# Kernel tuning notes

Measured on AMD Instinct MI355X. Metric: run time of the kernel, lower is better.

The kernel has to match this reference:

```python
import jax, jax.numpy as jnp
import numpy as np
from jax import lax
from jax.scipy.special import logsumexp

GW_WEIGHT = 20.0
GAMMA_P = 0.01
IN_ITER = 5
OUT_ITER = 10
LAMBDA_STEP = 0.01
N1, N2, D = 2048, 2048, 128
EMB_SCALE = 0.05  # keeps exp(-x@x.T) numerically sane, mimics trained embeddings
ADJ_DENSITY = 0.005


def setup_inputs() -> dict:
    key = jax.random.key(0)
    k1, k2, k3, k4 = jax.random.split(key, 4)
    out1 = jax.random.normal(k1, (N1, D), jnp.float32) * EMB_SCALE
    out2 = jax.random.normal(k2, (N2, D), jnp.float32) * EMB_SCALE

    def make_adj(k, n):
        m = (jax.random.uniform(k, (n, n)) < ADJ_DENSITY).astype(jnp.float32)
        m = jnp.maximum(m, m.T)                      # symmetric, like to_dense_adj of undirected graph
        return m * (1.0 - jnp.eye(n, dtype=jnp.float32))

    adj1 = make_adj(k3, N1)
    adj2 = make_adj(k4, N2)
    threshold_lambda = jnp.float32(1.0 / (N1 * N2))  # init_lambda / (n1*n2)
    return {"out1": out1, "out2": out2, "adj1": adj1, "adj2": adj2,
            "threshold_lambda": threshold_lambda}


def sinkhorn_stable(inter_c, intra_c1, intra_c2, gw_weight, gamma_p, lam,
                    in_iter, out_iter):
    """Log-domain (stabilized) entropic GW Sinkhorn.
    Outer loop: linearize the GW cost around current plan s (shifted by lam);
    inner loop: stabilized Sinkhorn with uniform marginals."""
    n1, n2 = inter_c.shape
    dt = inter_c.dtype
    log_mu = jnp.full((n1,), -np.log(n1), dt)
    log_nu = jnp.full((n2,), -np.log(n2), dt)
    c1sq = intra_c1 ** 2
    c2sq = intra_c2 ** 2
    s0 = jnp.full((n1, n2), 1.0 / (n1 * n2), dt)

    def outer_body(_, s):
        s_hat = s - lam
        a = jnp.sum(s_hat, axis=1)                    # [n1]
        b = jnp.sum(s_hat, axis=0)                    # [n2]
        # GW cost linearization: c1^2 a 1^T + 1 b^T c2^2 - 2 c1 s c2^T
        gw_cost = ((c1sq @ a)[:, None] + (b @ c2sq)[None, :]
                   - 2.0 * (intra_c1 @ s_hat @ intra_c2.T))
        cost = inter_c + gw_weight * gw_cost
        K = -cost / gamma_p                           # log kernel

        def inner_body(_, uv):
            u, v = uv
            u = log_mu - logsumexp(K + v[None, :], axis=1)
            v = log_nu - logsumexp(K + u[:, None], axis=0)
            return (u, v)

        u, v = lax.fori_loop(0, in_iter, inner_body,
                             (jnp.zeros((n1,), dt), jnp.zeros((n2,), dt)))
        return jnp.exp(K + u[:, None] + v[None, :])

    return lax.fori_loop(0, out_iter, outer_body, s0)


def _update_lambda(inter_c, intra_c1, intra_c2, s, gw_weight):
    # mid = c1^2 @ 1 * n2 + 1 @ c2^2 * n1 - 2 c1 @ 1 @ c2^T is rank-structured;
    # compute sum(mid*s) and sum(mid) without materializing mid.
    n1, n2 = inter_c.shape
    c1sq = intra_c1 ** 2
    c2sq = intra_c2 ** 2
    r1sq = jnp.sum(c1sq, axis=1)      # rowsum of c1^2  [n1]
    c2s = jnp.sum(c2sq, axis=0)       # colsum of c2^2  [n2]
    rs1 = jnp.sum(intra_c1, axis=1)   # [n1]
    rs2 = jnp.sum(intra_c2, axis=1)   # [n2]
    a_s = jnp.sum(s, axis=1)
    b_s = jnp.sum(s, axis=0)
    k1 = jnp.sum(inter_c)
    k2 = n2 * (r1sq @ a_s) + n1 * (c2s @ b_s) - 2.0 * (rs1 @ (s @ rs2))
    k3 = (n2 * n2) * jnp.sum(r1sq) + (n1 * n1) * jnp.sum(c2s) \
         - 2.0 * jnp.sum(rs1) * jnp.sum(rs2)
    return (k1 + 2.0 * gw_weight * k2) / (2.0 * gw_weight * k3)


def reference(out1, out2, adj1, adj2, threshold_lambda):
    n1, n2 = out1.shape[0], out2.shape[0]
    inter_c = jnp.exp(-(out1 @ out2.T))
    intra_c1 = jnp.exp(-(out1 @ out1.T)) * adj1
    intra_c2 = jnp.exp(-(out2 @ out2.T)) * adj2

    # torch.no_grad() block
    s = sinkhorn_stable(inter_c, intra_c1, intra_c2, GW_WEIGHT, GAMMA_P,
                        threshold_lambda, IN_ITER, OUT_ITER)
    lam = (LAMBDA_STEP * _update_lambda(inter_c, intra_c1, intra_c2, s, GW_WEIGHT)
           + (1.0 - LAMBDA_STEP) * threshold_lambda)

    s_hat = s - lam
    w_loss = jnp.sum(inter_c * s_hat)
    a = jnp.sum(s_hat, axis=1)
    b = jnp.sum(s_hat, axis=0)
    c1sq = intra_c1 ** 2
    c2sq = intra_c2 ** 2
    gw_loss = jnp.sum(((c1sq @ a)[:, None] + (b @ c2sq)[None, :]
                       - 2.0 * (intra_c1 @ s_hat @ intra_c2.T)) * s_hat)
    loss = w_loss + GW_WEIGHT * gw_loss + 20.0
    return (loss, s, lam)
```

## Files before the change

kernel.cpp:

```cpp
#include <hip/hip_runtime.h>
#include <math.h>

#define N 2048
#define DIM 128
#define CAP (N*64)
#define LOGN 7.6246189861593985f

typedef unsigned long long u64;
typedef unsigned int u32;
typedef unsigned short u16;

__device__ __forceinline__ u32 bf16bits(float f) {
  u32 x = __float_as_uint(f);
  return (x + 0x7fffu + ((x >> 16) & 1u)) >> 16;
}
__device__ __forceinline__ u32 pack_bf16x2(float lo, float hi) {
  return bf16bits(lo) | (bf16bits(hi) << 16);
}
__device__ __forceinline__ float bflo(u32 u) { return __uint_as_float(u << 16); }
__device__ __forceinline__ float bfhi(u32 u) { return __uint_as_float(u & 0xffff0000u); }


__global__ __launch_bounds__(256) void k_gemm_inter(
    const float* __restrict__ A, const float* __restrict__ B,
    float* __restrict__ O, double* __restrict__ k1p) {
  __shared__ __align__(16) float As[64][65];
  __shared__ __align__(16) float Bs[64][65];
  __shared__ float red[256];
  const int t = threadIdx.x;
  const int i0 = blockIdx.y * 64, j0 = blockIdx.x * 64;
  const int tx = t & 15, ty = t >> 4;
  float acc[4][4] = {};
  for (int kk = 0; kk < DIM; kk += 64) {
    if (kk) __syncthreads();
    for (int q = t; q < 64 * 16; q += 256) {
      int row = q >> 4, k4 = (q & 15) << 2;
      float4 av = *(const float4*)&A[(size_t)(i0 + row) * DIM + kk + k4];
      As[k4 + 0][row] = av.x; As[k4 + 1][row] = av.y;
      As[k4 + 2][row] = av.z; As[k4 + 3][row] = av.w;
      float4 bv = *(const float4*)&B[(size_t)(j0 + row) * DIM + kk + k4];
      Bs[k4 + 0][row] = bv.x; Bs[k4 + 1][row] = bv.y;
      Bs[k4 + 2][row] = bv.z; Bs[k4 + 3][row] = bv.w;
    }
    __syncthreads();
    #pragma unroll 4
    for (int k = 0; k < 64; ++k) {
      float av[4], bv[4];
      #pragma unroll
      for (int d = 0; d < 4; ++d) { av[d] = As[k][ty * 4 + d]; bv[d] = Bs[k][tx * 4 + d]; }
      #pragma unroll
      for (int di = 0; di < 4; ++di)
        #pragma unroll
        for (int dj = 0; dj < 4; ++dj)
          acc[di][dj] = fmaf(av[di], bv[dj], acc[di][dj]);
    }
  }
  float psum = 0.f;
  #pragma unroll
  for (int di = 0; di < 4; ++di)
    #pragma unroll
    for (int dj = 0; dj < 4; ++dj) {
      float vv = __expf(-acc[di][dj]);
      O[(size_t)(i0 + ty * 4 + di) * N + (j0 + tx * 4 + dj)] = vv;
      psum += vv;
    }
  red[t] = psum; __syncthreads();
  for (int off = 128; off; off >>= 1) { if (t < off) red[t] += red[t + off]; __syncthreads(); }
  if (t == 0) k1p[blockIdx.y * 32 + blockIdx.x] = (double)red[0];
}

__global__ __launch_bounds__(256) void k_count(const float* __restrict__ adj, int* __restrict__ cnt) {
  int i = blockIdx.x * 4 + (threadIdx.x >> 6);
  int lane = threadIdx.x & 63;
  const float* row = adj + (size_t)i * N;
  int c = 0;
  for (int j = lane; j < N; j += 64) c += (row[j] != 0.f) ? 1 : 0;
  for (int off = 32; off; off >>= 1) c += __shfl_down(c, off);
  if (lane == 0) cnt[i] = c;
}

__global__ __launch_bounds__(256) void k_scan(const int* __restrict__ cnt, int* __restrict__ rp) {
  __shared__ int sums[256];
  int t = threadIdx.x;
  int local[8]; int run = 0;
  int base = t * 8;
  #pragma unroll
  for (int k = 0; k < 8; ++k) { local[k] = run; run += cnt[base + k]; }
  sums[t] = run; __syncthreads();
  for (int off = 1; off < 256; off <<= 1) {
    int val = (t >= off) ? sums[t - off] : 0;
    __syncthreads();
    sums[t] += val;
    __syncthreads();
  }
  int pre = (t == 0) ? 0 : sums[t - 1];
  #pragma unroll
  for (int k = 0; k < 8; ++k) rp[base + k] = pre + local[k];
  if (t == 255) rp[N] = sums[255];
}

__global__ __launch_bounds__(256) void k_fill(const float* __restrict__ adj, const int* __restrict__ rp,
                                              int* __restrict__ cols, int* __restrict__ rows) {
  int i = blockIdx.x * 4 + (threadIdx.x >> 6);
  int lane = threadIdx.x & 63;
  const float* row = adj + (size_t)i * N;
  int pos = rp[i];
  for (int j0 = 0; j0 < N; j0 += 64) {
    bool p = row[j0 + lane] != 0.f;
    u64 mask = __ballot(p);
    if (p) {
      int off = __popcll(mask & ((1ull << lane) - 1ull));
      cols[pos + off] = j0 + lane;
      rows[pos + off] = i;
    }
    pos += __popcll(mask);
  }
}

__global__ __launch_bounds__(256) void k_vals(const int* __restrict__ rp, const int* __restrict__ rows,
                                              const int* __restrict__ cols, float* __restrict__ vals,
                                              const float* __restrict__ emb) {
  int lane = threadIdx.x & 63;
  int total = rp[N];
  for (int p = blockIdx.x * 4 + (threadIdx.x >> 6); p < total; p += 8192) {
    int i = rows[p], k = cols[p];
    const float* ei = emb + (size_t)i * DIM;
    const float* ek = emb + (size_t)k * DIM;
    float s = ei[lane] * ek[lane] + ei[lane + 64] * ek[lane + 64];
    for (int off = 32; off; off >>= 1) s += __shfl_down(s, off);
    if (lane == 0) vals[p] = __expf(-s);
  }
}

__global__ __launch_bounds__(256) void k_rowstats(const int* __restrict__ rp, const float* __restrict__ vals,
                                                  float* __restrict__ rs, float* __restrict__ rsq) {
  int i = blockIdx.x * 4 + (threadIdx.x >> 6);
  int lane = threadIdx.x & 63;
  int p0 = rp[i], p1 = rp[i + 1];
  float s1 = 0.f, s2 = 0.f;
  for (int p = p0 + lane; p < p1; p += 64) { float w = vals[p]; s1 += w; s2 += w * w; }
  for (int off = 32; off; off >>= 1) { s1 += __shfl_down(s1, off); s2 += __shfl_down(s2, off); }
  if (lane == 0) { rs[i] = s1; rsq[i] = s2; }
}

template<int V>
__global__ __launch_bounds__(256) void k_spmmt(const int* __restrict__ rp, const int* __restrict__ cols,
                                               const float* __restrict__ vals, const u32* __restrict__ S,
                                               const float* __restrict__ af, const float* __restrict__ bf,
                                               u16* __restrict__ Out) {
  __shared__ int winc[512];
  __shared__ float winv[512];
  __shared__ int rb[5];
  const int t = threadIdx.x;
  const int tile = blockIdx.x & 3;
  const int cu = tile * 256 + t;
  const int i0 = (blockIdx.x >> 2) * 4;
  const int p0 = rp[i0];
  if (t < 5) rb[t] = rp[i0 + t] - p0;
  __syncthreads();
  const int nn = rb[4];
  for (int k = t; k < nn; k += 256) {
    int col = cols[p0 + k];
    winc[k] = col << 10;
    winv[k] = (V == 0) ? vals[p0 + k] * af[col] : vals[p0 + k];
  }
  __syncthreads();
  float alo[4], ahi[4];
  #pragma unroll
  for (int r = 0; r < 4; ++r) {
    int pe = rb[r + 1], p = rb[r];
    float l0 = 0.f, l1 = 0.f, h0 = 0.f, h1 = 0.f;
    for (; p + 1 < pe; p += 2) {
      u32 u0 = S[winc[p] + cu], u1 = S[winc[p + 1] + cu];
      l0 = fmaf(winv[p],     bflo(u0), l0);  h0 = fmaf(winv[p],     bfhi(u0), h0);
      l1 = fmaf(winv[p + 1], bflo(u1), l1);  h1 = fmaf(winv[p + 1], bfhi(u1), h1);
    }
    if (p < pe) {
      u32 u = S[winc[p] + cu];
      l0 = fmaf(winv[p], bflo(u), l0);  h0 = fmaf(winv[p], bfhi(u), h0);
    }
    alo[r] = l0 + l1; ahi[r] = h0 + h1;
  }
  const int c0 = cu * 2;
  if (V == 0) {
    float2 bv = *(const float2*)&bf[c0];
    #pragma unroll
    for (int r = 0; r < 4; ++r) { alo[r] *= bv.x; ahi[r] *= bv.y; }
  }
  u32* O32 = (u32*)Out;
  *(uint2*)&O32[(size_t)c0 * 1024 + (i0 >> 1)] =
      make_uint2(pack_bf16x2(alo[0], alo[1]), pack_bf16x2(alo[2], alo[3]));
  *(uint2*)&O32[(size_t)(c0 + 1) * 1024 + (i0 >> 1)] =
      make_uint2(pack_bf16x2(ahi[0], ahi[1]), pack_bf16x2(ahi[2], ahi[3]));
}

template<int MODE>
__global__ __launch_bounds__(256) void k_iter(
    u32* __restrict__ P,
    const float* __restrict__ inter, const u32* __restrict__ M32,
    const int* __restrict__ rp1, const int* __restrict__ cols1, const float* __restrict__ vals1,
    const float* __restrict__ r1sq, const float* __restrict__ rs1,
    const float* __restrict__ r2sq, const float* __restrict__ rs2,
    const float* __restrict__ lamp, const float* __restrict__ asv_in,
    const float* __restrict__ bvec, float* __restrict__ avec,
    float* __restrict__ part) {
  __shared__ u32 Pl[4 * 1024];
  __shared__ float bl[N];
  __shared__ float a4[4];
  const int t = threadIdx.x;
  const int r0 = blockIdx.x * 4;
  const int w = t >> 6, lane = t & 63;
  const int row = r0 + w;

  if (MODE == 0) {
    #pragma unroll
    for (int q = 0; q < 2; ++q) {
      int j = (q * 256 + t) * 4;
      *(float4*)&bl[j] = *(const float4*)&bvec[j];
    }
    #pragma unroll
    for (int q = 0; q < 4; ++q) {
      int g = (q * 256 + t) * 4;
      *(uint4*)&Pl[g] = *(const uint4*)&P[(size_t)r0 * 1024 + g];
    }
    __syncthreads();
    float y = 0.f;
    const u32* Pr = Pl + w * 1024;
    #pragma unroll
    for (int k = 0; k < 16; ++k) {
      int g = lane + k * 64;
      u32 u = Pr[g];
      y = fmaf(bflo(u), bl[2 * g], y);
      y = fmaf(bfhi(u), bl[2 * g + 1], y);
    }
    for (int off = 32; off; off >>= 1) y += __shfl_xor(y, off);
    if (lane == 0) { float aw = 1.f / (2048.f * y); a4[w] = aw; avec[row] = aw; }
  } else {
    const float lam = *lamp;
    const float f = 0.00048828125f - lam * 2048.f;
    float ai_, rli;
    if (MODE == 2) {
      ai_ = -2000.f * r1sq[row] * f;
      rli = 4000.f * rs1[row] * (2.384185791015625e-07f - lam);
    } else {
      int q0 = rp1[row], q1 = rp1[row + 1];
      float acc = 0.f;
      for (int p = q0 + lane; p < q1; p += 64) {
        float wv = vals1[p];
        acc = fmaf(wv * wv, asv_in[cols1[p]], acc);
      }
      for (int off = 32; off; off >>= 1) acc += __shfl_xor(acc, off);
      ai_ = -2000.f * (acc - lam * 2048.f * r1sq[row]);
      rli = -4000.f * lam * rs1[row];
    }
    const float bjf = -2000.f * f;
    float kv[32];
    float m = -INFINITY;
    const float* ir = inter + (size_t)row * N;
    const u32* mr = M32 + (size_t)row * 1024;
    #pragma unroll
    for (int q = 0; q < 8; ++q) {
      int j = lane * 4 + q * 256;
      float4 iv = *(const float4*)&ir[j];
      float4 rq = *(const float4*)&r2sq[j];
      float4 r2 = *(const float4*)&rs2[j];
      float k0 = fmaf(-100.f, iv.x, fmaf(bjf, rq.x, ai_ + rli * r2.x));
      float k1 = fmaf(-100.f, iv.y, fmaf(bjf, rq.y, ai_ + rli * r2.y));
      float k2 = fmaf(-100.f, iv.z, fmaf(bjf, rq.z, ai_ + rli * r2.z));
      float k3 = fmaf(-100.f, iv.w, fmaf(bjf, rq.w, ai_ + rli * r2.w));
      if (MODE == 1) {
        uint2 mu = *(const uint2*)&mr[j >> 1];
        k0 = fmaf(4000.f, bflo(mu.x), k0);
        k1 = fmaf(4000.f, bfhi(mu.x), k1);
        k2 = fmaf(4000.f, bflo(mu.y), k2);
        k3 = fmaf(4000.f, bfhi(mu.y), k3);
      }
      kv[q * 4 + 0] = k0; kv[q * 4 + 1] = k1; kv[q * 4 + 2] = k2; kv[q * 4 + 3] = k3;
      m = fmaxf(m, fmaxf(fmaxf(k0, k1), fmaxf(k2, k3)));
    }
    for (int off = 32; off; off >>= 1) m = fmaxf(m, __shfl_xor(m, off));
    float ss = 0.f;
    #pragma unroll
    for (int q = 0; q < 8; ++q) {
      float p0 = __expf(kv[q * 4 + 0] - m);
      float p1 = __expf(kv[q * 4 + 1] - m);
      float p2 = __expf(kv[q * 4 + 2] - m);
      float p3 = __expf(kv[q * 4 + 3] - m);
      ss += (p0 + p1) + (p2 + p3);
      u32 lo = pack_bf16x2(p0, p1), hi = pack_bf16x2(p2, p3);
      int g = lane * 2 + q * 128;
      Pl[w * 1024 + g] = lo; Pl[w * 1024 + g + 1] = hi;
      *(uint2*)&P[(size_t)row * 1024 + g] = make_uint2(lo, hi);
    }
    for (int off = 32; off; off >>= 1) ss += __shfl_xor(ss, off);
    if (lane == 0) { float aw = 1.f / (2048.f * ss); a4[w] = aw; avec[row] = aw; }
  }
  __syncthreads();
  const float a0 = a4[0], a1 = a4[1], a2 = a4[2], a3 = a4[3];
  #pragma unroll
  for (int k = 0; k < 4; ++k) {
    int g = k * 256 + t;
    u32 u0 = Pl[g], u1 = Pl[1024 + g], u2 = Pl[2048 + g], u3 = Pl[3072 + g];
    float zlo = bflo(u0) * a0 + bflo(u1) * a1 + bflo(u2) * a2 + bflo(u3) * a3;
    float zhi = bfhi(u0) * a0 + bfhi(u1) * a1 + bfhi(u2) * a2 + bfhi(u3) * a3;
    *(float2*)&part[(size_t)blockIdx.x * N + 2 * g] = make_float2(zlo, zhi);
  }
}

__global__ __launch_bounds__(256) void k_comb(const float* __restrict__ part, float* __restrict__ bvec) {
  __shared__ float pp[16][17];
  const int t = threadIdx.x;
  const int cl = t & 15, kg = t >> 4;
  const int c = blockIdx.x * 16 + cl;
  float z = 0.f;
  for (int k = kg * 32; k < kg * 32 + 32; ++k) z += part[(size_t)k * N + c];
  pp[kg][cl] = z;
  __syncthreads();
  if (t < 16) {
    float zz = 0.f;
    #pragma unroll
    for (int g = 0; g < 16; ++g) zz += pp[g][t];
    bvec[blockIdx.x * 16 + t] = 1.f / (2048.f * zz);
  }
}

__global__ __launch_bounds__(256) void k_rowfin(const u32* __restrict__ P, const float* __restrict__ bvec,
                                                const float* __restrict__ avec, float* __restrict__ as_) {
  __shared__ float bl[N];
  const int t = threadIdx.x;
  #pragma unroll
  for (int q = 0; q < 2; ++q) {
    int j = (q * 256 + t) * 4;
    *(float4*)&bl[j] = *(const float4*)&bvec[j];
  }
  __syncthreads();
  const int w = t >> 6, lane = t & 63;
  const int row = blockIdx.x * 4 + w;
  const u32* Pr = P + (size_t)row * 1024;
  float y = 0.f;
  #pragma unroll
  for (int k = 0; k < 16; ++k) {
    int g = lane + k * 64;
    u32 u = Pr[g];
    y = fmaf(bflo(u), bl[2 * g], y);
    y = fmaf(bfhi(u), bl[2 * g + 1], y);
  }
  for (int off = 32; off; off >>= 1) y += __shfl_xor(y, off);
  if (lane == 0) as_[row] = avec[row] * y;
}


__global__ __launch_bounds__(256) void k_prep2(
    const int* __restrict__ rp1, const int* __restrict__ cols1, const float* __restrict__ vals1,
    const float* __restrict__ r2sq, const float* __restrict__ as_,
    float* __restrict__ paf, float* __restrict__ pbf) {
  int g = blockIdx.x * 256 + threadIdx.x;
  if (g < N) {
    int p0 = rp1[g], p1 = rp1[g + 1];
    float acc = 0.f;
    for (int p = p0; p < p1; ++p) { float w = vals1[p]; acc = fmaf(w * w, as_[cols1[p]], acc); }
    paf[g] = acc;
  } else {
    int j = g - N;
    pbf[j] = r2sq[j] * 0.00048828125f;
  }
}

__global__ __launch_bounds__(256) void k_fstats(
    const float* __restrict__ inter, const u32* __restrict__ P, const u32* __restrict__ M32,
    const float* __restrict__ rs2, const float* __restrict__ avec, const float* __restrict__ bvec,
    float* __restrict__ sOut, float* __restrict__ sisr, float* __restrict__ yv,
    double* __restrict__ dotp) {
  __shared__ __align__(16) float r2[N];
  __shared__ __align__(16) float bl[N];
  __shared__ double redm[4];
  const int t = threadIdx.x;
  #pragma unroll
  for (int q = 0; q < 2; ++q) {
    int j = (q * 256 + t) * 4;
    *(float4*)&r2[j] = *(const float4*)&rs2[j];
    *(float4*)&bl[j] = *(const float4*)&bvec[j];
  }
  __syncthreads();
  const int w = t >> 6, lane = t & 63;
  const int row = blockIdx.x * 4 + w;
  const float av = avec[row];
  const float* ir = inter + (size_t)row * N;
  const u32* mr = M32 + (size_t)row * 1024;
  const u32* Pr = P + (size_t)row * 1024;
  float* sr = sOut + (size_t)row * N;
  float d1 = 0.f, d2 = 0.f;
  double dm = 0.0;
  #pragma unroll 4
  for (int k = 0; k < 16; ++k) {
    int g = lane + k * 64;
    int j = 2 * g;
    u32 u = Pr[g];
    u32 mu = mr[g];
    float s0 = bflo(u) * av * bl[j];
    float s1 = bfhi(u) * av * bl[j + 1];
    float2 iv = *(const float2*)&ir[j];
    sr[j] = s0; sr[j + 1] = s1;
    d1 += iv.x * s0 + iv.y * s1;
    d2 += s0 * r2[j] + s1 * r2[j + 1];
    dm += (double)(bflo(mu) * s0) + (double)(bfhi(mu) * s1);
  }
  for (int off = 32; off; off >>= 1) {
    d1 += __shfl_down(d1, off);
    d2 += __shfl_down(d2, off);
    dm += __shfl_down(dm, off);
  }
  if (lane == 0) { sisr[row] = d1; yv[row] = d2; redm[w] = dm; }
  __syncthreads();
  if (t == 0) dotp[blockIdx.x] = redm[0] + redm[1] + redm[2] + redm[3];
}

__global__ __launch_bounds__(256) void k_final(
    const float* __restrict__ paf, const float* __restrict__ pbf,
    const float* __restrict__ r1sq, const float* __restrict__ r2sq,
    const float* __restrict__ rs1, const float* __restrict__ rs2,
    const float* __restrict__ as_,
    const float* __restrict__ yv, const float* __restrict__ sisr,
    const double* __restrict__ k1p, const double* __restrict__ dotp,
    const float* __restrict__ lamp, float* __restrict__ out_loss, float* __restrict__ out_lam) {
  __shared__ double red[256];
  int t = threadIdx.x;
  auto dred = [&](double acc) -> double {
    red[t] = acc; __syncthreads();
    for (int off = 128; off; off >>= 1) { if (t < off) red[t] += red[t + off]; __syncthreads(); }
    double r = red[0]; __syncthreads();
    return r;
  };
  auto dotv = [&](const float* a, const float* b) -> double {
    double acc = 0.0;
    for (int k = t; k < N; k += 256) acc += (double)a[k] * (b ? (double)b[k] : 1.0);
    return dred(acc);
  };
  double k1a = 0.0;
  for (int k = t; k < 1024; k += 256) k1a += k1p[k];
  double k1 = dred(k1a);
  double sma = 0.0;
  for (int k = t; k < 512; k += 256) sma += dotp[k];
  double smfs = dred(sma);
  double paas = dotv(paf, as_);
  double pbbs = dotv(pbf, nullptr) * (1.0 / 2048.0);
  double r1as = dotv(r1sq, as_);
  double rs1y = dotv(rs1, yv);
  double sis  = dotv(sisr, nullptr);
  double sr1  = dotv(r1sq, nullptr);
  double sr2  = dotv(r2sq, nullptr);
  double ss1  = dotv(rs1, nullptr);
  double ss2  = dotv(rs2, nullptr);
  if (t == 0) {
    double c2bs = sr2 / 2048.0;
    double lam0 = (double)*lamp;
    double k2 = 2048.0 * r1as + 2048.0 * c2bs - 2.0 * rs1y;
    double k3 = 2048.0 * 2048.0 * (sr1 + sr2) - 2.0 * ss1 * ss2;
    double upd = (k1 + 40.0 * k2) / (40.0 * k3);
    double lamn = 0.01 * upd + 0.99 * lam0;
    double g1 = paas + pbbs - 2.0 * smfs;
    double wl = sis - lamn * k1;
    double gwl = g1 - 2.0 * lamn * k2 + lamn * lamn * k3;
    double loss = wl + 20.0 * gwl + 20.0;
    *out_loss = (float)loss;
    *out_lam = (float)lamn;
  }
}


extern "C" void kernel_launch(void* const* d_in, const int* in_sizes, int n_in,
                              void* d_out, int out_size, void* d_ws, size_t ws_size,
                              hipStream_t stream) {
  (void)in_sizes; (void)n_in; (void)out_size; (void)ws_size;
  const float* out1 = (const float*)d_in[0];
  const float* out2 = (const float*)d_in[1];
  const float* adj1 = (const float*)d_in[2];
  const float* adj2 = (const float*)d_in[3];
  const float* lamp = (const float*)d_in[4];
  float* o = (float*)d_out;
  float* sOut = o + 1;

  char* w = (char*)d_ws;
  size_t off = 0;
  auto alloc = [&](size_t bytes) -> void* {
    void* p = w + off;
    off = (off + bytes + 255) & ~(size_t)255;
    return p;
  };
  const size_t NNf = (size_t)N * N * sizeof(float);
  float* inter = (float*)alloc(NNf);
  u32*  Pbuf   = (u32*)alloc((size_t)N * 1024 * sizeof(u32));
  u16*  Tth    = (u16*)alloc((size_t)N * N * sizeof(u16));
  u16*  Mb16   = (u16*)alloc((size_t)N * N * sizeof(u16));
  int* rp1   = (int*)alloc((N + 1) * sizeof(int));
  int* rp2   = (int*)alloc((N + 1) * sizeof(int));
  int* cnt   = (int*)alloc(N * sizeof(int));
  int* cols1 = (int*)alloc(CAP * sizeof(int));
  int* rows1 = (int*)alloc(CAP * sizeof(int));
  int* cols2 = (int*)alloc(CAP * sizeof(int));
  int* rows2 = (int*)alloc(CAP * sizeof(int));
  float* vals1 = (float*)alloc(CAP * sizeof(float));
  float* vals2 = (float*)alloc(CAP * sizeof(float));
  float* r1sq = (float*)alloc(N * sizeof(float));
  float* rs1  = (float*)alloc(N * sizeof(float));
  float* r2sq = (float*)alloc(N * sizeof(float));
  float* rs2v = (float*)alloc(N * sizeof(float));
  float* asv  = (float*)alloc(N * sizeof(float));
  float* avec = (float*)alloc(N * sizeof(float));
  float* bvec = (float*)alloc(N * sizeof(float));
  float* yv   = (float*)alloc(N * sizeof(float));
  float* sisr = (float*)alloc(N * sizeof(float));
  float* paf  = (float*)alloc(N * sizeof(float));
  float* pbf  = (float*)alloc(N * sizeof(float));
  float* part = (float*)alloc((size_t)512 * N * sizeof(float));
  double* k1p = (double*)alloc(1024 * sizeof(double));
  double* dotp= (double*)alloc(512 * sizeof(double));

  dim3 b(256);

  k_gemm_inter<<<dim3(32, 32), b, 0, stream>>>(out1, out2, inter, k1p);
  k_count<<<512, b, 0, stream>>>(adj1, cnt);
  k_scan<<<1, b, 0, stream>>>(cnt, rp1);
  k_count<<<512, b, 0, stream>>>(adj2, cnt);
  k_scan<<<1, b, 0, stream>>>(cnt, rp2);
  k_fill<<<512, b, 0, stream>>>(adj1, rp1, cols1, rows1);
  k_fill<<<512, b, 0, stream>>>(adj2, rp2, cols2, rows2);
  k_vals<<<2048, b, 0, stream>>>(rp1, rows1, cols1, vals1, out1);
  k_vals<<<2048, b, 0, stream>>>(rp2, rows2, cols2, vals2, out2);
  k_rowstats<<<512, b, 0, stream>>>(rp1, vals1, rs1, r1sq);
  k_rowstats<<<512, b, 0, stream>>>(rp2, vals2, rs2v, r2sq);

  for (int t = 0; t < 10; ++t) {
    if (t > 0) {
      k_spmmt<0><<<2048, b, 0, stream>>>(rp1, cols1, vals1, Pbuf, avec, bvec, Tth);
      k_spmmt<1><<<2048, b, 0, stream>>>(rp2, cols2, vals2, (const u32*)Tth, nullptr, nullptr, Mb16);
      k_iter<1><<<512, b, 0, stream>>>(Pbuf, inter, (const u32*)Mb16, rp1, cols1, vals1,
                                       r1sq, rs1, r2sq, rs2v, lamp, asv, bvec, avec, part);
    } else {
      k_iter<2><<<512, b, 0, stream>>>(Pbuf, inter, (const u32*)Mb16, rp1, cols1, vals1,
                                       r1sq, rs1, r2sq, rs2v, lamp, asv, bvec, avec, part);
    }
    k_comb<<<128, b, 0, stream>>>(part, bvec);
    for (int r = 1; r < 5; ++r) {
      k_iter<0><<<512, b, 0, stream>>>(Pbuf, inter, (const u32*)Mb16, rp1, cols1, vals1,
                                       r1sq, rs1, r2sq, rs2v, lamp, asv, bvec, avec, part);
      k_comb<<<128, b, 0, stream>>>(part, bvec);
    }
    k_rowfin<<<512, b, 0, stream>>>(Pbuf, bvec, avec, asv);
  }

  k_spmmt<0><<<2048, b, 0, stream>>>(rp1, cols1, vals1, Pbuf, avec, bvec, Tth);
  k_spmmt<1><<<2048, b, 0, stream>>>(rp2, cols2, vals2, (const u32*)Tth, nullptr, nullptr, Mb16);
  k_prep2<<<16, b, 0, stream>>>(rp1, cols1, vals1, r2sq, asv, paf, pbf);
  k_fstats<<<512, b, 0, stream>>>(inter, Pbuf, (const u32*)Mb16, rs2v, avec, bvec, sOut, sisr, yv, dotp);
  k_final<<<1, b, 0, stream>>>(paf, pbf, r1sq, r2sq, rs1, rs2v, asv, yv, sisr,
                               k1p, dotp, lamp, o, o + 1 + (size_t)N * N);
}
```

Measured before the change: 1.037 ms.

## Precompute bf16 exp(-100*inter) factor, drop max pass, and merge small kernels

Measured after the change: 989.3 us. -4.6%, faster.

```diff
diff --git a/kernel.cpp b/kernel.cpp
--- a/kernel.cpp
+++ b/kernel.cpp
@@ -4,7 +4,6 @@
 #define N 2048
 #define DIM 128
 #define CAP (N*64)
-#define LOGN 7.6246189861593985f
 
 typedef unsigned long long u64;
 typedef unsigned int u32;
@@ -23,7 +22,7 @@
 
 __global__ __launch_bounds__(256) void k_gemm_inter(
     const float* __restrict__ A, const float* __restrict__ B,
-    float* __restrict__ O, double* __restrict__ k1p) {
+    u16* __restrict__ Ib, u16* __restrict__ Eb, double* __restrict__ k1p) {
   __shared__ __align__(16) float As[64][65];
   __shared__ __align__(16) float Bs[64][65];
   __shared__ float red[256];
@@ -57,20 +56,29 @@
   }
   float psum = 0.f;
   #pragma unroll
-  for (int di = 0; di < 4; ++di)
+  for (int di = 0; di < 4; ++di) {
+    float iv[4], ev[4];
     #pragma unroll
     for (int dj = 0; dj < 4; ++dj) {
-      float vv = __expf(-acc[di][dj]);
-      O[(size_t)(i0 + ty * 4 + di) * N + (j0 + tx * 4 + dj)] = vv;
-      psum += vv;
-    }
+      iv[dj] = __expf(-acc[di][dj]);
+      ev[dj] = __expf(fmaf(-100.f, iv[dj], 100.f));
+      psum += iv[dj];
+    }
+    size_t base = (size_t)(i0 + ty * 4 + di) * N + (j0 + tx * 4);
+    *(uint2*)&Ib[base] = make_uint2(pack_bf16x2(iv[0], iv[1]), pack_bf16x2(iv[2], iv[3]));
+    *(uint2*)&Eb[base] = make_uint2(pack_bf16x2(ev[0], ev[1]), pack_bf16x2(ev[2], ev[3]));
+  }
   red[t] = psum; __syncthreads();
   for (int off = 128; off; off >>= 1) { if (t < off) red[t] += red[t + off]; __syncthreads(); }
   if (t == 0) k1p[blockIdx.y * 32 + blockIdx.x] = (double)red[0];
 }
 
-__global__ __launch_bounds__(256) void k_count(const float* __restrict__ adj, int* __restrict__ cnt) {
-  int i = blockIdx.x * 4 + (threadIdx.x >> 6);
+__global__ __launch_bounds__(256) void k_count2(const float* __restrict__ adj1, const float* __restrict__ adj2,
+                                                int* __restrict__ cnt1, int* __restrict__ cnt2) {
+  int half = blockIdx.x >> 9;
+  const float* adj = half ? adj2 : adj1;
+  int* cnt = half ? cnt2 : cnt1;
+  int i = (blockIdx.x & 511) * 4 + (threadIdx.x >> 6);
   int lane = threadIdx.x & 63;
   const float* row = adj + (size_t)i * N;
   int c = 0;
@@ -79,7 +87,10 @@
   if (lane == 0) cnt[i] = c;
 }
 
-__global__ __launch_bounds__(256) void k_scan(const int* __restrict__ cnt, int* __restrict__ rp) {
+__global__ __launch_bounds__(256) void k_scan2(const int* __restrict__ cnt1, const int* __restrict__ cnt2,
+                                               int* __restrict__ rp1, int* __restrict__ rp2) {
+  const int* cnt = blockIdx.x ? cnt2 : cnt1;
+  int* rp = blockIdx.x ? rp2 : rp1;
   __shared__ int sums[256];
   int t = threadIdx.x;
   int local[8]; int run = 0;
@@ -99,9 +110,16 @@
   if (t == 255) rp[N] = sums[255];
 }
 
-__global__ __launch_bounds__(256) void k_fill(const float* __restrict__ adj, const int* __restrict__ rp,
-                                              int* __restrict__ cols, int* __restrict__ rows) {
-  int i = blockIdx.x * 4 + (threadIdx.x >> 6);
+__global__ __launch_bounds__(256) void k_fill2(const float* __restrict__ adj1, const float* __restrict__ adj2,
+                                               const int* __restrict__ rp1, const int* __restrict__ rp2,
+                                               int* __restrict__ cols1, int* __restrict__ rows1,
+                                               int* __restrict__ cols2, int* __restrict__ rows2) {
+  int half = blockIdx.x >> 9;
+  const float* adj = half ? adj2 : adj1;
+  const int* rp = half ? rp2 : rp1;
+  int* cols = half ? cols2 : cols1;
+  int* rows = half ? rows2 : rows1;
+  int i = (blockIdx.x & 511) * 4 + (threadIdx.x >> 6);
   int lane = threadIdx.x & 63;
   const float* row = adj + (size_t)i * N;
   int pos = rp[i];
@@ -117,12 +135,20 @@
   }
 }
 
-__global__ __launch_bounds__(256) void k_vals(const int* __restrict__ rp, const int* __restrict__ rows,
-                                              const int* __restrict__ cols, float* __restrict__ vals,
-                                              const float* __restrict__ emb) {
+__global__ __launch_bounds__(256) void k_vals2(
+    const int* __restrict__ rp1, const int* __restrict__ rows1, const int* __restrict__ cols1,
+    float* __restrict__ vals1, const float* __restrict__ emb1,
+    const int* __restrict__ rp2, const int* __restrict__ rows2, const int* __restrict__ cols2,
+    float* __restrict__ vals2, const float* __restrict__ emb2) {
+  int half = blockIdx.x >> 10;
+  const int* rp = half ? rp2 : rp1;
+  const int* rows = half ? rows2 : rows1;
+  const int* cols = half ? cols2 : cols1;
+  float* vals = half ? vals2 : vals1;
+  const float* emb = half ? emb2 : emb1;
   int lane = threadIdx.x & 63;
   int total = rp[N];
-  for (int p = blockIdx.x * 4 + (threadIdx.x >> 6); p < total; p += 8192) {
+  for (int p = (blockIdx.x & 1023) * 4 + (threadIdx.x >> 6); p < total; p += 4096) {
     int i = rows[p], k = cols[p];
     const float* ei = emb + (size_t)i * DIM;
     const float* ek = emb + (size_t)k * DIM;
@@ -132,9 +158,17 @@
   }
 }
 
-__global__ __launch_bounds__(256) void k_rowstats(const int* __restrict__ rp, const float* __restrict__ vals,
-                                                  float* __restrict__ rs, float* __restrict__ rsq) {
-  int i = blockIdx.x * 4 + (threadIdx.x >> 6);
+__global__ __launch_bounds__(256) void k_rowstats2(
+    const int* __restrict__ rp1, const float* __restrict__ vals1,
+    float* __restrict__ rs1, float* __restrict__ rsq1,
+    const int* __restrict__ rp2, const float* __restrict__ vals2,
+    float* __restrict__ rs2, float* __restrict__ rsq2) {
+  int half = blockIdx.x >> 9;
+  const int* rp = half ? rp2 : rp1;
+  const float* vals = half ? vals2 : vals1;
+  float* rs = half ? rs2 : rs1;
+  float* rsq = half ? rsq2 : rsq1;
+  int i = (blockIdx.x & 511) * 4 + (threadIdx.x >> 6);
   int lane = threadIdx.x & 63;
   int p0 = rp[i], p1 = rp[i + 1];
   float s1 = 0.f, s2 = 0.f;
@@ -143,15 +177,38 @@
   if (lane == 0) { rs[i] = s1; rsq[i] = s2; }
 }
 
-template<int V>
+template<int V, int FIN>
 __global__ __launch_bounds__(256) void k_spmmt(const int* __restrict__ rp, const int* __restrict__ cols,
                                                const float* __restrict__ vals, const u32* __restrict__ S,
                                                const float* __restrict__ af, const float* __restrict__ bf,
-                                               u16* __restrict__ Out) {
+                                               u16* __restrict__ Out, float* __restrict__ asv) {
   __shared__ int winc[512];
   __shared__ float winv[512];
   __shared__ int rb[5];
+  __shared__ float blf[N];
   const int t = threadIdx.x;
+  if (FIN && blockIdx.x >= 2048) {
+    #pragma unroll
+    for (int q = 0; q < 2; ++q) {
+      int j = (q * 256 + t) * 4;
+      *(float4*)&blf[j] = *(const float4*)&bf[j];
+    }
+    __syncthreads();
+    const int w = t >> 6, lane = t & 63;
+    const int row = (blockIdx.x - 2048) * 4 + w;
+    const u32* Pr = S + (size_t)row * 1024;
+    float y = 0.f;
+    #pragma unroll
+    for (int k = 0; k < 16; ++k) {
+      int g = lane + k * 64;
+      u32 u = Pr[g];
+      y = fmaf(bflo(u), blf[2 * g], y);
+      y = fmaf(bfhi(u), blf[2 * g + 1], y);
+    }
+    for (int off = 32; off; off >>= 1) y += __shfl_xor(y, off);
+    if (lane == 0) asv[row] = af[row] * y;
+    return;
+  }
   const int tile = blockIdx.x & 3;
   const int cu = tile * 256 + t;
   const int i0 = (blockIdx.x >> 2) * 4;
@@ -197,7 +254,7 @@
 template<int MODE>
 __global__ __launch_bounds__(256) void k_iter(
     u32* __restrict__ P,
-    const float* __restrict__ inter, const u32* __restrict__ M32,
+    const u32* __restrict__ E32, const u32* __restrict__ M32,
     const int* __restrict__ rp1, const int* __restrict__ cols1, const float* __restrict__ vals1,
     const float* __restrict__ r1sq, const float* __restrict__ rs1,
     const float* __restrict__ r2sq, const float* __restrict__ rs2,
@@ -254,38 +311,30 @@
       rli = -4000.f * lam * rs1[row];
     }
     const float bjf = -2000.f * f;
-    float kv[32];
-    float m = -INFINITY;
-    const float* ir = inter + (size_t)row * N;
+    float ss = 0.f;
+    const u32* er = E32 + (size_t)row * 1024;
     const u32* mr = M32 + (size_t)row * 1024;
     #pragma unroll
     for (int q = 0; q < 8; ++q) {
       int j = lane * 4 + q * 256;
-      float4 iv = *(const float4*)&ir[j];
+      uint2 eu = *(const uint2*)&er[j >> 1];
       float4 rq = *(const float4*)&r2sq[j];
       float4 r2 = *(const float4*)&rs2[j];
-      float k0 = fmaf(-100.f, iv.x, fmaf(bjf, rq.x, ai_ + rli * r2.x));
-      float k1 = fmaf(-100.f, iv.y, fmaf(bjf, rq.y, ai_ + rli * r2.y));
-      float k2 = fmaf(-100.f, iv.z, fmaf(bjf, rq.z, ai_ + rli * r2.z));
-      float k3 = fmaf(-100.f, iv.w, fmaf(bjf, rq.w, ai_ + rli * r2.w));
+      float d0 = fmaf(bjf, rq.x, fmaf(rli, r2.x, ai_));
+      float d1 = fmaf(bjf, rq.y, fmaf(rli, r2.y, ai_));
+      float d2 = fmaf(bjf, rq.z, fmaf(rli, r2.z, ai_));
+      float d3 = fmaf(bjf, rq.w, fmaf(rli, r2.w, ai_));
       if (MODE == 1) {
         uint2 mu = *(const uint2*)&mr[j >> 1];
-        k0 = fmaf(4000.f, bflo(mu.x), k0);
-        k1 = fmaf(4000.f, bfhi(mu.x), k1);
-        k2 = fmaf(4000.f, bflo(mu.y), k2);
-        k3 = fmaf(4000.f, bfhi(mu.y), k3);
+        d0 = fmaf(4000.f, bflo(mu.x), d0);
+        d1 = fmaf(4000.f, bfhi(mu.x), d1);
+        d2 = fmaf(4000.f, bflo(mu.y), d2);
+        d3 = fmaf(4000.f, bfhi(mu.y), d3);
       }
-      kv[q * 4 + 0] = k0; kv[q * 4 + 1] = k1; kv[q * 4 + 2] = k2; kv[q * 4 + 3] = k3;
-      m = fmaxf(m, fmaxf(fmaxf(k0, k1), fmaxf(k2, k3)));
-    }
-    for (int off = 32; off; off >>= 1) m = fmaxf(m, __shfl_xor(m, off));
-    float ss = 0.f;
-    #pragma unroll
-    for (int q = 0; q < 8; ++q) {
-      float p0 = __expf(kv[q * 4 + 0] - m);
-      float p1 = __expf(kv[q * 4 + 1] - m);
-      float p2 = __expf(kv[q * 4 + 2] - m);
-      float p3 = __expf(kv[q * 4 + 3] - m);
+      float p0 = bflo(eu.x) * __expf(d0);
+      float p1 = bfhi(eu.x) * __expf(d1);
+      float p2 = bflo(eu.y) * __expf(d2);
+      float p3 = bfhi(eu.y) * __expf(d3);
       ss += (p0 + p1) + (p2 + p3);
       u32 lo = pack_bf16x2(p0, p1), hi = pack_bf16x2(p2, p3);
       int g = lane * 2 + q * 128;
@@ -324,57 +373,32 @@
   }
 }
 
-__global__ __launch_bounds__(256) void k_rowfin(const u32* __restrict__ P, const float* __restrict__ bvec,
-                                                const float* __restrict__ avec, float* __restrict__ as_) {
-  __shared__ float bl[N];
-  const int t = threadIdx.x;
-  #pragma unroll
-  for (int q = 0; q < 2; ++q) {
-    int j = (q * 256 + t) * 4;
-    *(float4*)&bl[j] = *(const float4*)&bvec[j];
-  }
-  __syncthreads();
-  const int w = t >> 6, lane = t & 63;
-  const int row = blockIdx.x * 4 + w;
-  const u32* Pr = P + (size_t)row * 1024;
-  float y = 0.f;
-  #pragma unroll
-  for (int k = 0; k < 16; ++k) {
-    int g = lane + k * 64;
-    u32 u = Pr[g];
-    y = fmaf(bflo(u), bl[2 * g], y);
-    y = fmaf(bfhi(u), bl[2 * g + 1], y);
-  }
-  for (int off = 32; off; off >>= 1) y += __shfl_xor(y, off);
-  if (lane == 0) as_[row] = avec[row] * y;
-}
-
-
-__global__ __launch_bounds__(256) void k_prep2(
-    const int* __restrict__ rp1, const int* __restrict__ cols1, const float* __restrict__ vals1,
-    const float* __restrict__ r2sq, const float* __restrict__ as_,
-    float* __restrict__ paf, float* __restrict__ pbf) {
-  int g = blockIdx.x * 256 + threadIdx.x;
-  if (g < N) {
-    int p0 = rp1[g], p1 = rp1[g + 1];
-    float acc = 0.f;
-    for (int p = p0; p < p1; ++p) { float w = vals1[p]; acc = fmaf(w * w, as_[cols1[p]], acc); }
-    paf[g] = acc;
-  } else {
-    int j = g - N;
-    pbf[j] = r2sq[j] * 0.00048828125f;
-  }
-}
 
 __global__ __launch_bounds__(256) void k_fstats(
-    const float* __restrict__ inter, const u32* __restrict__ P, const u32* __restrict__ M32,
+    const u32* __restrict__ Ib, const u32* __restrict__ P, const u32* __restrict__ M32,
     const float* __restrict__ rs2, const float* __restrict__ avec, const float* __restrict__ bvec,
     float* __restrict__ sOut, float* __restrict__ sisr, float* __restrict__ yv,
-    double* __restrict__ dotp) {
+    double* __restrict__ dotp,
+    const int* __restrict__ rp1, const int* __restrict__ cols1, const float* __restrict__ vals1,
+    const float* __restrict__ r2sq, const float* __restrict__ asv,
+    float* __restrict__ paf, float* __restrict__ pbf) {
+  const int t = threadIdx.x;
+  if (blockIdx.x >= 512) {
+    int g = (blockIdx.x - 512) * 256 + t;
+    if (g < N) {
+      int p0 = rp1[g], p1 = rp1[g + 1];
+      float acc = 0.f;
+      for (int p = p0; p < p1; ++p) { float w = vals1[p]; acc = fmaf(w * w, asv[cols1[p]], acc); }
+      paf[g] = acc;
+    } else {
+      int j = g - N;
+      pbf[j] = r2sq[j] * 0.00048828125f;
+    }
+    return;
+  }
   __shared__ __align__(16) float r2[N];
   __shared__ __align__(16) float bl[N];
   __shared__ double redm[4];
-  const int t = threadIdx.x;
   #pragma unroll
   for (int q = 0; q < 2; ++q) {
     int j = (q * 256 + t) * 4;
@@ -385,7 +409,7 @@
   const int w = t >> 6, lane = t & 63;
   const int row = blockIdx.x * 4 + w;
   const float av = avec[row];
-  const float* ir = inter + (size_t)row * N;
+  const u32* ir = Ib + (size_t)row * 1024;
   const u32* mr = M32 + (size_t)row * 1024;
   const u32* Pr = P + (size_t)row * 1024;
   float* sr = sOut + (size_t)row * N;
@@ -397,11 +421,11 @@
     int j = 2 * g;
     u32 u = Pr[g];
     u32 mu = mr[g];
+    u32 iu = ir[g];
     float s0 = bflo(u) * av * bl[j];
     float s1 = bfhi(u) * av * bl[j + 1];
-    float2 iv = *(const float2*)&ir[j];
     sr[j] = s0; sr[j + 1] = s1;
-    d1 += iv.x * s0 + iv.y * s1;
+    d1 += bflo(iu) * s0 + bfhi(iu) * s1;
     d2 += s0 * r2[j] + s1 * r2[j + 1];
     dm += (double)(bflo(mu) * s0) + (double)(bfhi(mu) * s1);
   }
@@ -487,14 +511,15 @@
     off = (off + bytes + 255) & ~(size_t)255;
     return p;
   };
-  const size_t NNf = (size_t)N * N * sizeof(float);
-  float* inter = (float*)alloc(NNf);
+  u16*  Ib     = (u16*)alloc((size_t)N * N * sizeof(u16));
+  u16*  Eb     = (u16*)alloc((size_t)N * N * sizeof(u16));
   u32*  Pbuf   = (u32*)alloc((size_t)N * 1024 * sizeof(u32));
   u16*  Tth    = (u16*)alloc((size_t)N * N * sizeof(u16));
   u16*  Mb16   = (u16*)alloc((size_t)N * N * sizeof(u16));
   int* rp1   = (int*)alloc((N + 1) * sizeof(int));
   int* rp2   = (int*)alloc((N + 1) * sizeof(int));
-  int* cnt   = (int*)alloc(N * sizeof(int));
+  int* cnt1  = (int*)alloc(N * sizeof(int));
+  int* cnt2  = (int*)alloc(N * sizeof(int));
   int* cols1 = (int*)alloc(CAP * sizeof(int));
   int* rows1 = (int*)alloc(CAP * sizeof(int));
   int* cols2 = (int*)alloc(CAP * sizeof(int));
@@ -518,41 +543,35 @@
 
   dim3 b(256);
 
-  k_gemm_inter<<<dim3(32, 32), b, 0, stream>>>(out1, out2, inter, k1p);
-  k_count<<<512, b, 0, stream>>>(adj1, cnt);
-  k_scan<<<1, b, 0, stream>>>(cnt, rp1);
-  k_count<<<512, b, 0, stream>>>(adj2, cnt);
-  k_scan<<<1, b, 0, stream>>>(cnt, rp2);
-  k_fill<<<512, b, 0, stream>>>(adj1, rp1, cols1, rows1);
-  k_fill<<<512, b, 0, stream>>>(adj2, rp2, cols2, rows2);
-  k_vals<<<2048, b, 0, stream>>>(rp1, rows1, cols1, vals1, out1);
-  k_vals<<<2048, b, 0, stream>>>(rp2, rows2, cols2, vals2, out2);
-  k_rowstats<<<512, b, 0, stream>>>(rp1, vals1, rs1, r1sq);
-  k_rowstats<<<512, b, 0, stream>>>(rp2, vals2, rs2v, r2sq);
+  k_gemm_inter<<<dim3(32, 32), b, 0, stream>>>(out1, out2, Ib, Eb, k1p);
+  k_count2<<<1024, b, 0, stream>>>(adj1, adj2, cnt1, cnt2);
+  k_scan2<<<2, b, 0, stream>>>(cnt1, cnt2, rp1, rp2);
+  k_fill2<<<1024, b, 0, stream>>>(adj1, adj2, rp1, rp2, cols1, rows1, cols2, rows2);
+  k_vals2<<<2048, b, 0, stream>>>(rp1, rows1, cols1, vals1, out1, rp2, rows2, cols2, vals2, out2);
+  k_rowstats2<<<1024, b, 0, stream>>>(rp1, vals1, rs1, r1sq, rp2, vals2, rs2v, r2sq);
 
   for (int t = 0; t < 10; ++t) {
     if (t > 0) {
-      k_spmmt<0><<<2048, b, 0, stream>>>(rp1, cols1, vals1, Pbuf, avec, bvec, Tth);
-      k_spmmt<1><<<2048, b, 0, stream>>>(rp2, cols2, vals2, (const u32*)Tth, nullptr, nullptr, Mb16);
-      k_iter<1><<<512, b, 0, stream>>>(Pbuf, inter, (const u32*)Mb16, rp1, cols1, vals1,
+      k_spmmt<0, 1><<<2560, b, 0, stream>>>(rp1, cols1, vals1, Pbuf, avec, bvec, Tth, asv);
+      k_spmmt<1, 0><<<2048, b, 0, stream>>>(rp2, cols2, vals2, (const u32*)Tth, nullptr, nullptr, Mb16, nullptr);
+      k_iter<1><<<512, b, 0, stream>>>(Pbuf, (const u32*)Eb, (const u32*)Mb16, rp1, cols1, vals1,
                                        r1sq, rs1, r2sq, rs2v, lamp, asv, bvec, avec, part);
     } else {
-      k_iter<2><<<512, b, 0, stream>>>(Pbuf, inter, (const u32*)Mb16, rp1, cols1, vals1,
+      k_iter<2><<<512, b, 0, stream>>>(Pbuf, (const u32*)Eb, (const u32*)Mb16, rp1, cols1, vals1,
                                        r1sq, rs1, r2sq, rs2v, lamp, asv, bvec, avec, part);
     }
     k_comb<<<128, b, 0, stream>>>(part, bvec);
     for (int r = 1; r < 5; ++r) {
-      k_iter<0><<<512, b, 0, stream>>>(Pbuf, inter, (const u32*)Mb16, rp1, cols1, vals1,
+      k_iter<0><<<512, b, 0, stream>>>(Pbuf, (const u32*)Eb, (const u32*)Mb16, rp1, cols1, vals1,
                                        r1sq, rs1, r2sq, rs2v, lamp, asv, bvec, avec, part);
       k_comb<<<128, b, 0, stream>>>(part, bvec);
     }
-    k_rowfin<<<512, b, 0, stream>>>(Pbuf, bvec, avec, asv);
-  }
-
-  k_spmmt<0><<<2048, b, 0, stream>>>(rp1, cols1, vals1, Pbuf, avec, bvec, Tth);
-  k_spmmt<1><<<2048, b, 0, stream>>>(rp2, cols2, vals2, (const u32*)Tth, nullptr, nullptr, Mb16);
-  k_prep2<<<16, b, 0, stream>>>(rp1, cols1, vals1, r2sq, asv, paf, pbf);
-  k_fstats<<<512, b, 0, stream>>>(inter, Pbuf, (const u32*)Mb16, rs2v, avec, bvec, sOut, sisr, yv, dotp);
+  }
+
+  k_spmmt<0, 1><<<2560, b, 0, stream>>>(rp1, cols1, vals1, Pbuf, avec, bvec, Tth, asv);
+  k_spmmt<1, 0><<<2048, b, 0, stream>>>(rp2, cols2, vals2, (const u32*)Tth, nullptr, nullptr, Mb16, nullptr);
+  k_fstats<<<528, b, 0, stream>>>((const u32*)Ib, Pbuf, (const u32*)Mb16, rs2v, avec, bvec,
+                                  sOut, sisr, yv, dotp, rp1, cols1, vals1, r2sq, asv, paf, pbf);
   k_final<<<1, b, 0, stream>>>(paf, pbf, r1sq, r2sq, rs1, rs2v, asv, yv, sisr,
                                k1p, dotp, lamp, o, o + 1 + (size_t)N * N);
 }
```
